# Performance work log

Hardware: AMD Instinct MI355X
Metric: run time of the kernel (lower is better)

The kernel has to match this reference:

```python
import jax, jax.numpy as jnp
import numpy as np
import itertools

N_ELEC = 128
BOX_L = 10.0
DIM = 3
BATCH = 4096


def gen_kpoints(N, L, dim):
    # Faithful numpy port of genKpoints (FermiNet make_kpoints variant).
    rec = 2.0 * np.pi / L
    dk = 1.0 + 1e-05
    max_k = int((N * dk) ** (1.0 / dim) + 0.5)
    ordinals = sorted(range(-max_k, max_k + 1), key=abs)
    ords = np.array(list(itertools.product(ordinals, repeat=dim)), dtype=np.float64)
    kpoints = ords * rec
    order = np.argsort(np.linalg.norm(kpoints, axis=1), kind='stable')
    kpoints = kpoints[order]
    return kpoints[:N].astype(np.float32)


def make_switches(kpoints, dim):
    # Select cos for k-points on the 'positive' side, sin(-k.r) for the rest.
    weights = 10.0 ** np.arange(1, dim + 1)
    weighted_sums = np.sign(kpoints).dot(weights)
    k_signs = np.sign(weighted_sums + 1.0)
    cos_switch = ((k_signs + 1.0) / 2.0).astype(np.float32)
    sin_switch = ((1.0 - k_signs) / 2.0).astype(np.float32)
    return cos_switch, sin_switch


def setup_inputs() -> dict:
    key = jax.random.key(0)
    rs = jax.random.uniform(key, (BATCH, N_ELEC, DIM), dtype=jnp.float32) * BOX_L
    kpoints = gen_kpoints(N_ELEC, BOX_L, DIM)
    cos_switch, sin_switch = make_switches(kpoints, DIM)
    return {
        'rs': rs,
        'kpoints': jnp.asarray(kpoints),
        'cos_switch': jnp.asarray(cos_switch),
        'sin_switch': jnp.asarray(sin_switch),
    }


def reference(rs, kpoints, cos_switch, sin_switch):
    # dots[b, i, m] = k_m . r_{b,i}   -> [B, N, N]
    dots = jnp.einsum('bnd,md->bnm', rs, kpoints)
    # Slater matrix: rows = particles, cols = plane-wave orbitals.
    slater = cos_switch * jnp.cos(dots) + sin_switch * jnp.sin(-dots)
    # log |det| per walker (batched LU) -> [B]
    return jnp.linalg.slogdet(slater)[1]
```

## Files before the change

kernel.cpp:

```cpp
#include <hip/hip_runtime.h>
#include <stdint.h>

#define NM 128
#define NT 512

typedef float v2f __attribute__((ext_vector_type(2)));

__device__ __forceinline__ float readlane_f(float v, int lane) {
    return __int_as_float(__builtin_amdgcn_readlane(__float_as_int(v), lane));
}

__device__ __forceinline__ unsigned wave_max_dpp(unsigned x) {
    int v = (int)x;
#define DPP_STEP(ctrl) \
    { int o = __builtin_amdgcn_update_dpp(0, v, ctrl, 0xf, 0xf, true); \
      v = ((unsigned)o > (unsigned)v) ? o : v; }
    DPP_STEP(0x111)
    DPP_STEP(0x112)
    DPP_STEP(0x114)
    DPP_STEP(0x118)
    DPP_STEP(0x142)
    DPP_STEP(0x143)
#undef DPP_STEP
    return (unsigned)v;
}

__device__ __forceinline__ unsigned pack_key(float v, int r) {
    return (((__float_as_uint(v) & 0x7fffffffu) >> 6) << 7) | (unsigned)r;
}

__device__ __forceinline__ unsigned argmax_bcast(unsigned ka, unsigned kb) {
    const unsigned m = wave_max_dpp(ka > kb ? ka : kb);
    return (unsigned)__builtin_amdgcn_readlane((int)m, 63);
}

__device__ __forceinline__ float sel_readlane(v2f c, int p) {
    return (p < 64) ? readlane_f(c.x, p) : readlane_f(c.y, p - 64);
}

template<int B, int N>
__device__ __forceinline__ void extract_apply(v2f (&sv)[16], int p, v2f lm) {
    float u[N];
    if (p < 64) {
#pragma unroll
        for (int j = 0; j < N; ++j) u[j] = readlane_f(sv[B + j].x, p);
    } else {
#pragma unroll
        for (int j = 0; j < N; ++j) u[j] = readlane_f(sv[B + j].y, p - 64);
    }
#pragma unroll
    for (int j = 0; j < N; ++j)
        sv[B + j] = __builtin_elementwise_fma((v2f){-u[j], -u[j]}, lm, sv[B + j]);
}

template<int B>
__device__ __forceinline__ void lookahead8(v2f (&sv)[16], bool& elim0, bool& elim1,
                                           int r0, int r1, int l, int g,
                                           float2 (*colvg)[64],
                                           unsigned* keysF, float* pivsF,
                                           ulonglong2* masks) {
    const bool e0in = elim0, e1in = elim1;
#pragma unroll
    for (int i = 0; i < 8; ++i) {
        const v2f c = sv[B + i];
        const unsigned key = argmax_bcast(elim0 ? 0u : pack_key(c.x, r0),
                                          elim1 ? 0u : pack_key(c.y, r1));
        const int pu = __builtin_amdgcn_readfirstlane((int)(key & 127u));
        const float piv = sel_readlane(c, pu);
        const float rcp = __builtin_amdgcn_rcpf(piv);
        elim0 = elim0 || (r0 == pu);
        elim1 = elim1 || (r1 == pu);
        const v2f lm = { elim0 ? 0.0f : c.x * rcp,
                         elim1 ? 0.0f : c.y * rcp };
        colvg[i][l] = make_float2(lm.x, lm.y);
#pragma unroll
        for (int m = i + 1; m < 8; ++m) {
            const float u = sel_readlane(sv[B + m], pu);
            sv[B + m] = __builtin_elementwise_fma((v2f){-u, -u}, lm, sv[B + m]);
        }
        if (l == 0) { keysF[8 * g + i] = key; pivsF[8 * g + i] = piv; }
    }
    const unsigned long long b0 = __ballot(elim0 && !e0in);
    const unsigned long long b1 = __ballot(elim1 && !e1in);
    if (l == 0) masks[g] = make_ulonglong2(b0, b1);
}

__global__ __launch_bounds__(NT, 6)
void slater_logdet(const float* __restrict__ rs,
                   const float* __restrict__ kpts,
                   const float* __restrict__ csw,
                   const float* __restrict__ ssw,
                   float* __restrict__ out) {
    __shared__ float2 colv[2][8][64];
    __shared__ unsigned keysF[NM];
    __shared__ float    pivsF[NM];
    __shared__ ulonglong2 masks[NM / 8];
    __shared__ float    redf[2];

    const int t  = threadIdx.x;
    const int b  = blockIdx.x;
    const int w  = t >> 6;
    const int l  = t & 63;
    const int c0 = w << 4;
    const int r0 = l, r1 = l + 64;

    v2f sv[16];
    {
        const float x0 = rs[(b * NM + r0) * 3 + 0];
        const float y0 = rs[(b * NM + r0) * 3 + 1];
        const float z0 = rs[(b * NM + r0) * 3 + 2];
        const float x1 = rs[(b * NM + r1) * 3 + 0];
        const float y1 = rs[(b * NM + r1) * 3 + 1];
        const float z1 = rs[(b * NM + r1) * 3 + 2];
#pragma unroll
        for (int j = 0; j < 16; ++j) {
            const int m = c0 + j;
            const float kx = kpts[m * 3 + 0], ky = kpts[m * 3 + 1], kz = kpts[m * 3 + 2];
            const float cw = csw[m], sw = ssw[m];
            float sn, cn;
            __sincosf(kx * x0 + ky * y0 + kz * z0, &sn, &cn);
            sv[j].x = cw * cn - sw * sn;
            __sincosf(kx * x1 + ky * y1 + kz * z1, &sn, &cn);
            sv[j].y = cw * cn - sw * sn;
        }
    }

    bool elim0 = false, elim1 = false;

    if (w == 0)
        lookahead8<0>(sv, elim0, elim1, r0, r1, l, 0, colv[0], keysF, pivsF, masks);
    __syncthreads();

    const int liveEnd = (2 * w < 14) ? 2 * w : 14;
    int rd = 0;
    for (; rd <= liveEnd; ++rd) {
        const uint4 ka = *(const uint4*)&keysF[8 * rd];
        const uint4 kb = *(const uint4*)&keysF[8 * rd + 4];
        const int p0 = __builtin_amdgcn_readfirstlane((int)(ka.x & 127u));
        const int p1 = __builtin_amdgcn_readfirstlane((int)(ka.y & 127u));
        const int p2 = __builtin_amdgcn_readfirstlane((int)(ka.z & 127u));
        const int p3 = __builtin_amdgcn_readfirstlane((int)(ka.w & 127u));
        const int p4 = __builtin_amdgcn_readfirstlane((int)(kb.x & 127u));
        const int p5 = __builtin_amdgcn_readfirstlane((int)(kb.y & 127u));
        const int p6 = __builtin_amdgcn_readfirstlane((int)(kb.z & 127u));
        const int p7 = __builtin_amdgcn_readfirstlane((int)(kb.w & 127u));
        const ulonglong2 mk = masks[rd];
        elim0 = elim0 || (((mk.x >> l) & 1ull) != 0);
        elim1 = elim1 || (((mk.y >> l) & 1ull) != 0);

        const int par = rd & 1;
        const float2 la0 = colv[par][0][l];
        const float2 la1 = colv[par][1][l];
        const float2 la2 = colv[par][2][l];
        const float2 la3 = colv[par][3][l];
        const float2 la4 = colv[par][4][l];
        const float2 la5 = colv[par][5][l];
        const float2 la6 = colv[par][6][l];
        const float2 la7 = colv[par][7][l];

        if (rd < 2 * w) {
            extract_apply<0, 8>(sv, p0, (v2f){la0.x, la0.y});
            extract_apply<8, 8>(sv, p0, (v2f){la0.x, la0.y});
            extract_apply<0, 8>(sv, p1, (v2f){la1.x, la1.y});
            extract_apply<8, 8>(sv, p1, (v2f){la1.x, la1.y});
            extract_apply<0, 8>(sv, p2, (v2f){la2.x, la2.y});
            extract_apply<8, 8>(sv, p2, (v2f){la2.x, la2.y});
            extract_apply<0, 8>(sv, p3, (v2f){la3.x, la3.y});
            extract_apply<8, 8>(sv, p3, (v2f){la3.x, la3.y});
            extract_apply<0, 8>(sv, p4, (v2f){la4.x, la4.y});
            extract_apply<8, 8>(sv, p4, (v2f){la4.x, la4.y});
            extract_apply<0, 8>(sv, p5, (v2f){la5.x, la5.y});
            extract_apply<8, 8>(sv, p5, (v2f){la5.x, la5.y});
            extract_apply<0, 8>(sv, p6, (v2f){la6.x, la6.y});
            extract_apply<8, 8>(sv, p6, (v2f){la6.x, la6.y});
            extract_apply<0, 8>(sv, p7, (v2f){la7.x, la7.y});
            extract_apply<8, 8>(sv, p7, (v2f){la7.x, la7.y});
        } else {
            extract_apply<8, 8>(sv, p0, (v2f){la0.x, la0.y});
            extract_apply<8, 8>(sv, p1, (v2f){la1.x, la1.y});
            extract_apply<8, 8>(sv, p2, (v2f){la2.x, la2.y});
            extract_apply<8, 8>(sv, p3, (v2f){la3.x, la3.y});
            extract_apply<8, 8>(sv, p4, (v2f){la4.x, la4.y});
            extract_apply<8, 8>(sv, p5, (v2f){la5.x, la5.y});
            extract_apply<8, 8>(sv, p6, (v2f){la6.x, la6.y});
            extract_apply<8, 8>(sv, p7, (v2f){la7.x, la7.y});
        }

        if (rd == 2 * w - 1)
            lookahead8<0>(sv, elim0, elim1, r0, r1, l, rd + 1,
                          colv[(rd + 1) & 1], keysF, pivsF, masks);
        if (rd == 2 * w)
            lookahead8<8>(sv, elim0, elim1, r0, r1, l, rd + 1,
                          colv[(rd + 1) & 1], keysF, pivsF, masks);

        __syncthreads();
    }
    for (; rd < 15; ++rd) __syncthreads();

    float lg = 0.0f;
    if (t < NM) {
        lg = __logf(fabsf(pivsF[t]));
#pragma unroll
        for (int off = 32; off > 0; off >>= 1)
            lg += __shfl_xor(lg, off, 64);
        if ((t & 63) == 0) redf[t >> 6] = lg;
    }
    __syncthreads();
    if (t == 0) out[b] = redf[0] + redf[1];
}

extern "C" void kernel_launch(void* const* d_in, const int* in_sizes, int n_in,
                              void* d_out, int out_size, void* d_ws, size_t ws_size,
                              hipStream_t stream) {
    const float* rs = (const float*)d_in[0];
    const float* kp = (const float*)d_in[1];
    const float* cs = (const float*)d_in[2];
    const float* ss = (const float*)d_in[3];
    float* out = (float*)d_out;
    const int batch = in_sizes[0] / (NM * 3);
    slater_logdet<<<dim3(batch), dim3(NT), 0, stream>>>(rs, kp, cs, ss, out);
}
```

Baseline: 400.8 us.

## Halve threads per block; each wave owns 32 columns of the Slater matrix

The block shrinks from 8 to 4 waves, and each wave now holds 32 columns in registers instead of 16. The blocked LU schedule is rewritten so each wave runs four lookahead panels and applies updates only to its still-live column groups. This cuts the number of barriers-sharing waves and may improve per-wave ILP. In exchange it doubles register pressure, lowers the launch_bounds occupancy hint, and serialises more work per wave, which reduces parallelism within each block.

Result: slower. 512.4 us (+27.8%).

```diff
diff --git a/kernel.cpp b/kernel.cpp
--- a/kernel.cpp
+++ b/kernel.cpp
@@ -2,7 +2,7 @@
 #include <stdint.h>
 
 #define NM 128
-#define NT 512
+#define NT 256
 
 typedef float v2f __attribute__((ext_vector_type(2)));
 
@@ -38,23 +38,35 @@
     return (p < 64) ? readlane_f(c.x, p) : readlane_f(c.y, p - 64);
 }
 
-template<int B, int N>
-__device__ __forceinline__ void extract_apply(v2f (&sv)[16], int p, v2f lm) {
-    float u[N];
+template<int B>
+__device__ __forceinline__ void extract_apply8(v2f (&sv)[32], int p, v2f lm) {
+    float u[8];
     if (p < 64) {
 #pragma unroll
-        for (int j = 0; j < N; ++j) u[j] = readlane_f(sv[B + j].x, p);
+        for (int j = 0; j < 8; ++j) u[j] = readlane_f(sv[B + j].x, p);
     } else {
 #pragma unroll
-        for (int j = 0; j < N; ++j) u[j] = readlane_f(sv[B + j].y, p - 64);
-    }
-#pragma unroll
-    for (int j = 0; j < N; ++j)
+        for (int j = 0; j < 8; ++j) u[j] = readlane_f(sv[B + j].y, p - 64);
+    }
+#pragma unroll
+    for (int j = 0; j < 8; ++j)
         sv[B + j] = __builtin_elementwise_fma((v2f){-u[j], -u[j]}, lm, sv[B + j]);
 }
 
+template<int B0>
+__device__ __forceinline__ void applyFrom(v2f (&sv)[32], const int (&p)[8],
+                                          const v2f (&lm)[8]) {
+#pragma unroll
+    for (int i = 0; i < 8; ++i) {
+        if (B0 <= 0) extract_apply8<0 >(sv, p[i], lm[i]);
+        if (B0 <= 1) extract_apply8<8 >(sv, p[i], lm[i]);
+        if (B0 <= 2) extract_apply8<16>(sv, p[i], lm[i]);
+        if (B0 <= 3) extract_apply8<24>(sv, p[i], lm[i]);
+    }
+}
+
 template<int B>
-__device__ __forceinline__ void lookahead8(v2f (&sv)[16], bool& elim0, bool& elim1,
+__device__ __forceinline__ void lookahead8(v2f (&sv)[32], bool& elim0, bool& elim1,
                                            int r0, int r1, int l, int g,
                                            float2 (*colvg)[64],
                                            unsigned* keysF, float* pivsF,
@@ -85,7 +97,7 @@
     if (l == 0) masks[g] = make_ulonglong2(b0, b1);
 }
 
-__global__ __launch_bounds__(NT, 6)
+__global__ __launch_bounds__(NT, 4)
 void slater_logdet(const float* __restrict__ rs,
                    const float* __restrict__ kpts,
                    const float* __restrict__ csw,
@@ -101,10 +113,10 @@
     const int b  = blockIdx.x;
     const int w  = t >> 6;
     const int l  = t & 63;
-    const int c0 = w << 4;
+    const int c0 = w << 5;
     const int r0 = l, r1 = l + 64;
 
-    v2f sv[16];
+    v2f sv[32];
     {
         const float x0 = rs[(b * NM + r0) * 3 + 0];
         const float y0 = rs[(b * NM + r0) * 3 + 1];
@@ -113,7 +125,7 @@
         const float y1 = rs[(b * NM + r1) * 3 + 1];
         const float z1 = rs[(b * NM + r1) * 3 + 2];
 #pragma unroll
-        for (int j = 0; j < 16; ++j) {
+        for (int j = 0; j < 32; ++j) {
             const int m = c0 + j;
             const float kx = kpts[m * 3 + 0], ky = kpts[m * 3 + 1], kz = kpts[m * 3 + 2];
             const float cw = csw[m], sw = ssw[m];
@@ -131,68 +143,54 @@
         lookahead8<0>(sv, elim0, elim1, r0, r1, l, 0, colv[0], keysF, pivsF, masks);
     __syncthreads();
 
-    const int liveEnd = (2 * w < 14) ? 2 * w : 14;
+    const int base    = 4 * w - 1;
+    const int liveEnd = (4 * w + 2 < 14) ? 4 * w + 2 : 14;
     int rd = 0;
     for (; rd <= liveEnd; ++rd) {
         const uint4 ka = *(const uint4*)&keysF[8 * rd];
         const uint4 kb = *(const uint4*)&keysF[8 * rd + 4];
-        const int p0 = __builtin_amdgcn_readfirstlane((int)(ka.x & 127u));
-        const int p1 = __builtin_amdgcn_readfirstlane((int)(ka.y & 127u));
-        const int p2 = __builtin_amdgcn_readfirstlane((int)(ka.z & 127u));
-        const int p3 = __builtin_amdgcn_readfirstlane((int)(ka.w & 127u));
-        const int p4 = __builtin_amdgcn_readfirstlane((int)(kb.x & 127u));
-        const int p5 = __builtin_amdgcn_readfirstlane((int)(kb.y & 127u));
-        const int p6 = __builtin_amdgcn_readfirstlane((int)(kb.z & 127u));
-        const int p7 = __builtin_amdgcn_readfirstlane((int)(kb.w & 127u));
+        int p[8];
+        p[0] = __builtin_amdgcn_readfirstlane((int)(ka.x & 127u));
+        p[1] = __builtin_amdgcn_readfirstlane((int)(ka.y & 127u));
+        p[2] = __builtin_amdgcn_readfirstlane((int)(ka.z & 127u));
+        p[3] = __builtin_amdgcn_readfirstlane((int)(ka.w & 127u));
+        p[4] = __builtin_amdgcn_readfirstlane((int)(kb.x & 127u));
+        p[5] = __builtin_amdgcn_readfirstlane((int)(kb.y & 127u));
+        p[6] = __builtin_amdgcn_readfirstlane((int)(kb.z & 127u));
+        p[7] = __builtin_amdgcn_readfirstlane((int)(kb.w & 127u));
         const ulonglong2 mk = masks[rd];
         elim0 = elim0 || (((mk.x >> l) & 1ull) != 0);
         elim1 = elim1 || (((mk.y >> l) & 1ull) != 0);
 
         const int par = rd & 1;
-        const float2 la0 = colv[par][0][l];
-        const float2 la1 = colv[par][1][l];
-        const float2 la2 = colv[par][2][l];
-        const float2 la3 = colv[par][3][l];
-        const float2 la4 = colv[par][4][l];
-        const float2 la5 = colv[par][5][l];
-        const float2 la6 = colv[par][6][l];
-        const float2 la7 = colv[par][7][l];
-
-        if (rd < 2 * w) {
-            extract_apply<0, 8>(sv, p0, (v2f){la0.x, la0.y});
-            extract_apply<8, 8>(sv, p0, (v2f){la0.x, la0.y});
-            extract_apply<0, 8>(sv, p1, (v2f){la1.x, la1.y});
-            extract_apply<8, 8>(sv, p1, (v2f){la1.x, la1.y});
-            extract_apply<0, 8>(sv, p2, (v2f){la2.x, la2.y});
-            extract_apply<8, 8>(sv, p2, (v2f){la2.x, la2.y});
-            extract_apply<0, 8>(sv, p3, (v2f){la3.x, la3.y});
-            extract_apply<8, 8>(sv, p3, (v2f){la3.x, la3.y});
-            extract_apply<0, 8>(sv, p4, (v2f){la4.x, la4.y});
-            extract_apply<8, 8>(sv, p4, (v2f){la4.x, la4.y});
-            extract_apply<0, 8>(sv, p5, (v2f){la5.x, la5.y});
-            extract_apply<8, 8>(sv, p5, (v2f){la5.x, la5.y});
-            extract_apply<0, 8>(sv, p6, (v2f){la6.x, la6.y});
-            extract_apply<8, 8>(sv, p6, (v2f){la6.x, la6.y});
-            extract_apply<0, 8>(sv, p7, (v2f){la7.x, la7.y});
-            extract_apply<8, 8>(sv, p7, (v2f){la7.x, la7.y});
+        v2f lm[8];
+#pragma unroll
+        for (int i = 0; i < 8; ++i) {
+            const float2 la = colv[par][i][l];
+            lm[i] = (v2f){la.x, la.y};
+        }
+
+        const int d = rd - base;
+        if (d < 0) {
+            applyFrom<0>(sv, p, lm);
+        } else if (d == 0) {
+            applyFrom<0>(sv, p, lm);
+            lookahead8<0 >(sv, elim0, elim1, r0, r1, l, rd + 1,
+                           colv[(rd + 1) & 1], keysF, pivsF, masks);
+        } else if (d == 1) {
+            applyFrom<1>(sv, p, lm);
+            lookahead8<8 >(sv, elim0, elim1, r0, r1, l, rd + 1,
+                           colv[(rd + 1) & 1], keysF, pivsF, masks);
+        } else if (d == 2) {
+            applyFrom<2>(sv, p, lm);
+            lookahead8<16>(sv, elim0, elim1, r0, r1, l, rd + 1,
+                           colv[(rd + 1) & 1], keysF, pivsF, masks);
         } else {
-            extract_apply<8, 8>(sv, p0, (v2f){la0.x, la0.y});
-            extract_apply<8, 8>(sv, p1, (v2f){la1.x, la1.y});
-            extract_apply<8, 8>(sv, p2, (v2f){la2.x, la2.y});
-            extract_apply<8, 8>(sv, p3, (v2f){la3.x, la3.y});
-            extract_apply<8, 8>(sv, p4, (v2f){la4.x, la4.y});
-            extract_apply<8, 8>(sv, p5, (v2f){la5.x, la5.y});
-            extract_apply<8, 8>(sv, p6, (v2f){la6.x, la6.y});
-            extract_apply<8, 8>(sv, p7, (v2f){la7.x, la7.y});
-        }
-
-        if (rd == 2 * w - 1)
-            lookahead8<0>(sv, elim0, elim1, r0, r1, l, rd + 1,
-                          colv[(rd + 1) & 1], keysF, pivsF, masks);
-        if (rd == 2 * w)
-            lookahead8<8>(sv, elim0, elim1, r0, r1, l, rd + 1,
-                          colv[(rd + 1) & 1], keysF, pivsF, masks);
-
+            applyFrom<3>(sv, p, lm);
+            if (rd + 1 < 16)
+                lookahead8<24>(sv, elim0, elim1, r0, r1, l, rd + 1,
+                               colv[(rd + 1) & 1], keysF, pivsF, masks);
+        }
         __syncthreads();
     }
     for (; rd < 15; ++rd) __syncthreads();
```
